# Kernel optimization log

Hardware: AMD Instinct MI355X
Metric: run time of the kernel (lower is better)

The kernel has to match this reference:

```python
import jax, jax.numpy as jnp
import numpy as np

N_V, N_H, T, B = 1024, 512, 128, 256


def setup_inputs() -> dict:
    key = jax.random.key(0)
    k = jax.random.split(key, 3)
    v_data = (jax.random.uniform(k[0], (N_V, T, B)) < 0.5).astype(jnp.float32)  # binary visibles
    W = 0.01 * jax.random.normal(k[1], (N_H, N_V), jnp.float32)
    U = 0.01 * jax.random.normal(k[2], (N_H, N_H), jnp.float32)
    b_h = jnp.zeros((N_H,), jnp.float32)
    b_init = jnp.zeros((N_H,), jnp.float32)
    b_v = jnp.zeros((N_V,), jnp.float32)
    return {"v_data": v_data, "W": W, "U": U, "b_h": b_h, "b_init": b_init,
            "b_v": b_v, "CDk": 2}


def _sample_r_over_time(v, W, U, b_h, b_init):
    # v: (V,T,B) -> r: (H,T,B). Sequential mean-field recurrence over T
    # (RTRBM._sample_r_given_v_over_time: t=0 uses b_init and U=0, t>0 uses U,b_h).
    Wv = jnp.einsum('hv,vtb->thb', W, v)  # (T,H,B)
    r0 = jax.nn.sigmoid(Wv[0] + b_init[:, None])

    def step(r_lag, wv_t):
        r_t = jax.nn.sigmoid(wv_t + U @ r_lag + b_h[:, None])
        return r_t, r_t

    _, rs = jax.lax.scan(step, r0, Wv[1:])
    r = jnp.concatenate([r0[None], rs], axis=0)  # (T,H,B)
    return jnp.transpose(r, (1, 0, 2))  # (H,T,B)


def _parallel_r(v, r_lagged, W, U, b_h, b_init):
    # RTRBM._parallel_sample_r_h_given_v probabilities; v:(V,T,B), r_lagged:(H,T,B)
    r0 = jax.nn.sigmoid(jnp.einsum('hv,vb->hb', W, v[:, 0]) + b_init[:, None])
    rr = jax.nn.sigmoid(jnp.einsum('hv,vtb->htb', W, v[:, 1:])
                        + jnp.einsum('hr,rtb->htb', U, r_lagged[:, :-1])
                        + b_h[:, None, None])
    return jnp.concatenate([r0[:, None], rr], axis=1)  # (H,T,B)


def reference(v_data, W, U, b_h, b_init, b_v, CDk):
    key = jax.random.key(42)
    r_data = _sample_r_over_time(v_data, W, U, b_h, b_init)
    key, sk = jax.random.split(key)
    h_model = jax.random.bernoulli(sk, _parallel_r(v_data, r_data, W, U, b_h, b_init)).astype(v_data.dtype)
    for _ in range(CDk - 1):  # CD-k Gibbs chain (CDk is a concrete Python int)
        key, k1, k2 = jax.random.split(key, 3)
        v_prob = jax.nn.sigmoid(jnp.einsum('hv,htb->vtb', W, h_model) + b_v[:, None, None])
        v_model = jax.random.bernoulli(k1, v_prob).astype(v_data.dtype)
        h_model = jax.random.bernoulli(k2, _parallel_r(v_model, r_data, W, U, b_h, b_init)).astype(v_data.dtype)
    key, kf = jax.random.split(key)
    v_model = jax.random.bernoulli(
        kf, jax.nn.sigmoid(jnp.einsum('hv,htb->vtb', W, h_model) + b_v[:, None, None])
    ).astype(v_data.dtype)
    return (v_model, r_data)
```

## Files before the change

kernel.cpp:

```cpp
#include <hip/hip_runtime.h>
#include <stdint.h>

typedef unsigned long long u64;
typedef uint32_t u32;

#define NV 1024
#define NH 512
#define TT 128
#define BB 256
#define TBsz (TT*BB)
#define HTBsz (NH*TBsz)
#define VTBsz (NV*TBsz)
#define NWV (NV/64)
#define NWH (NH/64)
#define QCAP 1048576u
#define DELTA 5e-4

__host__ __device__ inline void tf2x32(uint32_t k0, uint32_t k1,
                                       uint32_t x0, uint32_t x1,
                                       uint32_t& o0, uint32_t& o1) {
  const uint32_t ks2 = k0 ^ k1 ^ 0x1BD11BDAu;
#define ROTL(x,d) (((x)<<(d))|((x)>>(32-(d))))
#define RND(r) { x0 += x1; x1 = ROTL(x1,r); x1 ^= x0; }
  x0 += k0;  x1 += k1;
  RND(13) RND(15) RND(26) RND(6)
  x0 += k1;  x1 += ks2 + 1u;
  RND(17) RND(29) RND(16) RND(24)
  x0 += ks2; x1 += k0 + 2u;
  RND(13) RND(15) RND(26) RND(6)
  x0 += k0;  x1 += k1 + 3u;
  RND(17) RND(29) RND(16) RND(24)
  x0 += k1;  x1 += ks2 + 4u;
  RND(13) RND(15) RND(26) RND(6)
  x0 += ks2; x1 += k0 + 5u;
  o0 = x0; o1 = x1;
#undef RND
#undef ROTL
}

__device__ inline double tf_uniform64(uint32_t k0, uint32_t k1, uint32_t i) {
  uint32_t o0, o1;
  tf2x32(k0, k1, 0u, i, o0, o1);
  uint32_t bits = o0 ^ o1;
  uint32_t fb = (bits >> 9) | 0x3f800000u;
  float f = __uint_as_float(fb) - 1.0f;
  return (double)f;
}

__device__ inline double sigmoid64(double x) { return 1.0 / (1.0 + exp(-x)); }

__global__ __launch_bounds__(256) void kcvt(const float* __restrict__ s,
                                            double* __restrict__ d, int n) {
  int i = blockIdx.x * 256 + threadIdx.x;
  if (i < n) d[i] = (double)s[i];
}

__global__ __launch_bounds__(256) void kprepU(const float* __restrict__ U,
                                              float4* __restrict__ UB) {
  int i = blockIdx.x * 256 + threadIdx.x;
  int r4 = i / NH;
  int h  = i % NH;
  const float* __restrict__ p = U + (size_t)h*NH + r4*4;
  UB[i] = make_float4(p[0], p[1], p[2], p[3]);
}

__global__ __launch_bounds__(256) void kprepUT(const float* __restrict__ U,
                                               float* __restrict__ UT) {
  int i = blockIdx.x * 256 + threadIdx.x;
  int r = i / NH;
  int h = i % NH;
  UT[i] = U[(size_t)h*NH + r];
}

__global__ __launch_bounds__(256) void kpack_f32(const float* __restrict__ in,
                                                 u64* __restrict__ out) {
  int tb = blockIdx.x * 256 + threadIdx.x;
  for (int w = 0; w < NWV; ++w) {
    u64 m = 0;
    #pragma unroll 8
    for (int j = 0; j < 64; ++j)
      m |= (u64)(in[(size_t)(w*64 + j)*TBsz + tb] != 0.0f ? 1 : 0) << j;
    out[(size_t)tb*NWV + w] = m;
  }
}

__global__ __launch_bounds__(256) void kWv(const u64* __restrict__ vb,
                                           const double* __restrict__ W64,
                                           double* __restrict__ WvT) {
  const int HM = 8;
  int t  = blockIdx.x / (NH/HM);
  int h0 = (blockIdx.x % (NH/HM)) * HM;
  int tb = t*BB + threadIdx.x;
  u64 m[NWV];
  #pragma unroll
  for (int w = 0; w < NWV; ++w) m[w] = vb[(size_t)tb*NWV + w];
  double acc[HM];
  #pragma unroll
  for (int i = 0; i < HM; ++i) acc[i] = 0.0;
  const double2* __restrict__ W2 = (const double2*)W64;
  for (int w = 0; w < NWV; ++w) {
    u64 mw = m[w];
    #pragma unroll 8
    for (int j2 = 0; j2 < 32; ++j2) {
      double bd0 = (double)((unsigned)((mw >> (2*j2+0)) & 1ull));
      double bd1 = (double)((unsigned)((mw >> (2*j2+1)) & 1ull));
      int vi = w*32 + j2;
      #pragma unroll
      for (int i = 0; i < HM; ++i) {
        double2 wv = W2[(size_t)(h0+i)*(NV/2) + vi];
        acc[i] = fma(bd0, wv.x, acc[i]);
        acc[i] = fma(bd1, wv.y, acc[i]);
      }
    }
  }
  #pragma unroll
  for (int i = 0; i < HM; ++i)
    WvT[(size_t)tb*NH + h0 + i] = acc[i];
}

__global__ __launch_bounds__(512) void krecur(const double* __restrict__ WvT,
                                              const float4* __restrict__ UB,
                                              const float* __restrict__ bh,
                                              const float* __restrict__ binit,
                                              double* __restrict__ rT) {
  __shared__ double rA[2][NH];
  const int b = blockIdx.x;
  const int h = threadIdx.x;
  const double bhd = (double)bh[h];
  double p = sigmoid64(WvT[(size_t)b*NH + h] + (double)binit[h]);
  rA[0][h] = p;
  rT[(size_t)b*NH + h] = p;
  __syncthreads();
  int cur = 0;
  for (int t = 1; t < TT; ++t) {
    double acc = WvT[((size_t)t*BB + b)*NH + h];
    double a0=0, a1=0, a2=0, a3=0;
    const double2* __restrict__ rA2 = (const double2*)rA[cur];
    #pragma unroll 4
    for (int r = 0; r < NH; r += 4) {
      float4 u4 = UB[(size_t)(r >> 2)*NH + h];
      double2 q01 = rA2[(r>>1)+0];
      double2 q23 = rA2[(r>>1)+1];
      a0 = fma((double)u4.x, q01.x, a0);
      a1 = fma((double)u4.y, q01.y, a1);
      a2 = fma((double)u4.z, q23.x, a2);
      a3 = fma((double)u4.w, q23.y, a3);
    }
    p = sigmoid64((acc + ((a0+a1)+(a2+a3))) + bhd);
    rA[cur ^ 1][h] = p;
    rT[((size_t)t*BB + b)*NH + h] = p;
    __syncthreads();
    cur ^= 1;
  }
}

__global__ __launch_bounds__(256) void ktrans(const double* __restrict__ rT,
                                              float* __restrict__ out_r) {
  __shared__ double lds[32][33];
  int t  = blockIdx.x;
  int h0 = blockIdx.y * 32;
  int b0 = blockIdx.z * 32;
  int tx = threadIdx.x & 31;
  int ty = threadIdx.x >> 5;
  #pragma unroll
  for (int i = 0; i < 4; ++i) {
    int row = ty*4 + i;
    lds[row][tx] = rT[((size_t)t*BB + b0 + row)*NH + h0 + tx];
  }
  __syncthreads();
  #pragma unroll
  for (int i = 0; i < 4; ++i) {
    int row = ty*4 + i;
    out_r[(size_t)(h0+row)*TBsz + (size_t)t*BB + b0 + tx] = (float)lds[tx][row];
  }
}

__global__ __launch_bounds__(256) void ksample8(const double* __restrict__ rT,
                                                uint8_t* __restrict__ hbytes,
                                                u32 k0, u32 k1) {
  int i  = blockIdx.x * 256 + threadIdx.x;
  int tb = i >> 6;
  int hw = i & 63;
  int t = tb / BB, b = tb % BB;
  const double* __restrict__ rp = rT + ((size_t)t*BB + b)*NH + hw*8;
  unsigned byte = 0;
  #pragma unroll
  for (int j = 0; j < 8; ++j) {
    double p = rp[j];
    double u = tf_uniform64(k0, k1, (u32)((hw*8 + j)*TBsz + tb));
    byte |= (u < p) ? (1u << j) : 0u;
  }
  hbytes[(size_t)tb*(NH/8) + hw] = (uint8_t)byte;
}

__global__ __launch_bounds__(256) void kvis32(
    const float* __restrict__ W, const float* __restrict__ bv,
    const u64* __restrict__ hbits, uint8_t* __restrict__ vbytes,
    float* __restrict__ vf, u32* __restrict__ queue, u32* __restrict__ cnt,
    u32 k0, u32 k1) {
  const int VM = 16;
  int t  = blockIdx.x / (NV/VM);
  int v0 = (blockIdx.x % (NV/VM)) * VM;
  int tb = t*BB + threadIdx.x;
  u64 hb[NWH];
  #pragma unroll
  for (int w = 0; w < NWH; ++w) hb[w] = hbits[(size_t)tb*NWH + w];
  float acc[VM];
  #pragma unroll
  for (int i = 0; i < VM; ++i) acc[i] = 0.f;
  for (int w = 0; w < NWH; ++w) {
    u64 mw = hb[w];
    #pragma unroll 4
    for (int j = 0; j < 64; ++j) {
      float bd = (float)((u32)((mw >> j) & 1ull));
      const float4* __restrict__ Wp4 =
          (const float4*)(W + (size_t)(w*64 + j)*NV + v0);
      float4 w0 = Wp4[0], w1 = Wp4[1], w2 = Wp4[2], w3 = Wp4[3];
      acc[ 0] = fmaf(bd, w0.x, acc[ 0]);
      acc[ 1] = fmaf(bd, w0.y, acc[ 1]);
      acc[ 2] = fmaf(bd, w0.z, acc[ 2]);
      acc[ 3] = fmaf(bd, w0.w, acc[ 3]);
      acc[ 4] = fmaf(bd, w1.x, acc[ 4]);
      acc[ 5] = fmaf(bd, w1.y, acc[ 5]);
      acc[ 6] = fmaf(bd, w1.z, acc[ 6]);
      acc[ 7] = fmaf(bd, w1.w, acc[ 7]);
      acc[ 8] = fmaf(bd, w2.x, acc[ 8]);
      acc[ 9] = fmaf(bd, w2.y, acc[ 9]);
      acc[10] = fmaf(bd, w2.z, acc[10]);
      acc[11] = fmaf(bd, w2.w, acc[11]);
      acc[12] = fmaf(bd, w3.x, acc[12]);
      acc[13] = fmaf(bd, w3.y, acc[13]);
      acc[14] = fmaf(bd, w3.z, acc[14]);
      acc[15] = fmaf(bd, w3.w, acc[15]);
    }
  }
  unsigned bits = 0;
  #pragma unroll
  for (int i = 0; i < VM; ++i) {
    float p = 1.f / (1.f + __expf(-(acc[i] + bv[v0+i])));
    size_t o = (size_t)(v0+i)*TBsz + tb;
    double u = tf_uniform64(k0, k1, (u32)o);
    double diff = (double)p - u;
    unsigned smp = diff > 0.0 ? 1u : 0u;
    if (fabs(diff) < DELTA) {
      u32 s = atomicAdd(cnt, 1u);
      if (s < QCAP) queue[s] = (u32)o;
    }
    bits |= smp << i;
    if (vf) vf[o] = (float)smp;
  }
  if (vbytes)
    *(uint16_t*)(vbytes + (size_t)tb*(NV/8) + (v0 >> 3)) = (uint16_t)bits;
}

__global__ __launch_bounds__(256) void kvis_fix(
    const float* __restrict__ W, const float* __restrict__ bv,
    const u64* __restrict__ hbits, u64* __restrict__ fixbits,
    float* __restrict__ vf, const u32* __restrict__ queue,
    const u32* __restrict__ cnt, u32 k0, u32 k1) {
  u32 n = *cnt; if (n > QCAP) n = QCAP;
  for (u32 q = blockIdx.x*256 + threadIdx.x; q < n; q += gridDim.x*256) {
    u32 o = queue[q];
    u32 v = o / TBsz, tb = o % TBsz;
    double a0=0, a1=0, a2=0, a3=0;
    for (int w = 0; w < NWH; ++w) {
      u64 mw = hbits[(size_t)tb*NWH + w];
      for (int j = 0; j < 64; j += 4) {
        if ((mw >> (j+0)) & 1ull) a0 += (double)W[(size_t)(w*64+j+0)*NV + v];
        if ((mw >> (j+1)) & 1ull) a1 += (double)W[(size_t)(w*64+j+1)*NV + v];
        if ((mw >> (j+2)) & 1ull) a2 += (double)W[(size_t)(w*64+j+2)*NV + v];
        if ((mw >> (j+3)) & 1ull) a3 += (double)W[(size_t)(w*64+j+3)*NV + v];
      }
    }
    double p = sigmoid64(((a0+a1)+(a2+a3)) + (double)bv[v]);
    double u = tf_uniform64(k0, k1, o);
    unsigned smp = (u < p) ? 1u : 0u;
    if (vf) vf[o] = (float)smp;
    if (fixbits) {
      size_t wi = (size_t)tb*NWV + (v >> 6);
      unsigned bit = v & 63u;
      unsigned cur = (unsigned)((fixbits[wi] >> bit) & 1ull);
      if (cur != smp) atomicXor(&fixbits[wi], 1ull << bit);
    }
  }
}

__global__ __launch_bounds__(256) void khid32(
    const u64* __restrict__ vbits, const float* __restrict__ W,
    const float* __restrict__ UT, const float* __restrict__ bh,
    const float* __restrict__ binit, const float* __restrict__ r32,
    uint8_t* __restrict__ hbytes, u32* __restrict__ queue,
    u32* __restrict__ cnt, u32 k0, u32 k1) {
  const int HM = 8;
  int t  = blockIdx.x / (NH/HM);
  int h0 = (blockIdx.x % (NH/HM)) * HM;
  int tb = t*BB + threadIdx.x;
  u64 m[NWV];
  #pragma unroll
  for (int w = 0; w < NWV; ++w) m[w] = vbits[(size_t)tb*NWV + w];
  float acc[HM];
  #pragma unroll
  for (int i = 0; i < HM; ++i) acc[i] = 0.f;
  const float4* __restrict__ W4 = (const float4*)W;
  for (int w = 0; w < NWV; ++w) {
    u64 mw = m[w];
    #pragma unroll 4
    for (int j4 = 0; j4 < 16; ++j4) {
      float bd0 = (float)((u32)((mw >> (4*j4+0)) & 1ull));
      float bd1 = (float)((u32)((mw >> (4*j4+1)) & 1ull));
      float bd2 = (float)((u32)((mw >> (4*j4+2)) & 1ull));
      float bd3 = (float)((u32)((mw >> (4*j4+3)) & 1ull));
      int vi = w*16 + j4;
      #pragma unroll
      for (int i = 0; i < HM; ++i) {
        float4 wv = W4[(size_t)(h0+i)*(NV/4) + vi];
        acc[i] = fmaf(bd0, wv.x, acc[i]);
        acc[i] = fmaf(bd1, wv.y, acc[i]);
        acc[i] = fmaf(bd2, wv.z, acc[i]);
        acc[i] = fmaf(bd3, wv.w, acc[i]);
      }
    }
  }
  if (t > 0) {
    const float* __restrict__ rp = r32 + (size_t)(t-1)*BB + threadIdx.x;
    const float4* __restrict__ UT4 = (const float4*)UT;
    #pragma unroll 4
    for (int r = 0; r < NH; ++r) {
      float rv = rp[(size_t)r*TBsz];
      float4 ua = UT4[(size_t)r*(NH/4) + (h0 >> 2) + 0];
      float4 ub = UT4[(size_t)r*(NH/4) + (h0 >> 2) + 1];
      acc[0] = fmaf(ua.x, rv, acc[0]);
      acc[1] = fmaf(ua.y, rv, acc[1]);
      acc[2] = fmaf(ua.z, rv, acc[2]);
      acc[3] = fmaf(ua.w, rv, acc[3]);
      acc[4] = fmaf(ub.x, rv, acc[4]);
      acc[5] = fmaf(ub.y, rv, acc[5]);
      acc[6] = fmaf(ub.z, rv, acc[6]);
      acc[7] = fmaf(ub.w, rv, acc[7]);
    }
    #pragma unroll
    for (int i = 0; i < HM; ++i) acc[i] += bh[h0+i];
  } else {
    #pragma unroll
    for (int i = 0; i < HM; ++i) acc[i] += binit[h0+i];
  }
  unsigned byte = 0;
  #pragma unroll
  for (int i = 0; i < HM; ++i) {
    float p = 1.f / (1.f + __expf(-acc[i]));
    size_t o = (size_t)(h0+i)*TBsz + tb;
    double u = tf_uniform64(k0, k1, (u32)o);
    double diff = (double)p - u;
    unsigned smp = diff > 0.0 ? 1u : 0u;
    if (fabs(diff) < DELTA) {
      u32 s = atomicAdd(cnt, 1u);
      if (s < QCAP) queue[s] = (u32)o;
    }
    byte |= smp << i;
  }
  hbytes[(size_t)tb*(NH/8) + (h0 >> 3)] = (uint8_t)byte;
}

__global__ __launch_bounds__(256) void khid_fix(
    const u64* __restrict__ vbits, const float* __restrict__ W,
    const double* __restrict__ U64, const float* __restrict__ bh,
    const float* __restrict__ binit, const double* __restrict__ rT,
    u64* __restrict__ fixbits, const u32* __restrict__ queue,
    const u32* __restrict__ cnt, u32 k0, u32 k1) {
  u32 n = *cnt; if (n > QCAP) n = QCAP;
  for (u32 q = blockIdx.x*256 + threadIdx.x; q < n; q += gridDim.x*256) {
    u32 o = queue[q];
    u32 h = o / TBsz, tb = o % TBsz;
    u32 t = tb / BB, b = tb % BB;
    double a0=0, a1=0, a2=0, a3=0;
    for (int w = 0; w < NWV; ++w) {
      u64 mw = vbits[(size_t)tb*NWV + w];
      for (int j = 0; j < 64; j += 4) {
        if ((mw >> (j+0)) & 1ull) a0 += (double)W[(size_t)h*NV + w*64+j+0];
        if ((mw >> (j+1)) & 1ull) a1 += (double)W[(size_t)h*NV + w*64+j+1];
        if ((mw >> (j+2)) & 1ull) a2 += (double)W[(size_t)h*NV + w*64+j+2];
        if ((mw >> (j+3)) & 1ull) a3 += (double)W[(size_t)h*NV + w*64+j+3];
      }
    }
    double logit = (a0+a1) + (a2+a3);
    if (t > 0) {
      const double* __restrict__ rp = rT + ((size_t)(t-1)*BB + b)*NH;
      const double* __restrict__ Ur = U64 + (size_t)h*NH;
      double u0=0, u1=0, u2=0, u3=0;
      for (int r = 0; r < NH; r += 4) {
        u0 = fma(Ur[r+0], rp[r+0], u0);
        u1 = fma(Ur[r+1], rp[r+1], u1);
        u2 = fma(Ur[r+2], rp[r+2], u2);
        u3 = fma(Ur[r+3], rp[r+3], u3);
      }
      logit = (logit + ((u0+u1)+(u2+u3))) + (double)bh[h];
    } else {
      logit += (double)binit[h];
    }
    double p = sigmoid64(logit);
    double u = tf_uniform64(k0, k1, o);
    unsigned smp = (u < p) ? 1u : 0u;
    size_t wi = (size_t)tb*NWH + (h >> 6);
    unsigned bit = h & 63u;
    unsigned cur = (unsigned)((fixbits[wi] >> bit) & 1ull);
    if (cur != smp) atomicXor(&fixbits[wi], 1ull << bit);
  }
}

extern "C" void kernel_launch(void* const* d_in, const int* in_sizes, int n_in,
                              void* d_out, int out_size, void* d_ws, size_t ws_size,
                              hipStream_t stream) {
  const float* vd    = (const float*)d_in[0];
  const float* W     = (const float*)d_in[1];
  const float* U     = (const float*)d_in[2];
  const float* bh    = (const float*)d_in[3];
  const float* binit = (const float*)d_in[4];
  const float* bv    = (const float*)d_in[5];

  float* out_v = (float*)d_out;
  float* out_r = (float*)d_out + VTBsz;
  double* WvT = (double*)d_out;

  char* w = (char*)d_ws;
  double* rT    = (double*)w;  w += (size_t)HTBsz*8;
  u64* vdbits   = (u64*)w;     w += (size_t)TBsz*NWV*8;
  u64* v1bits   = (u64*)w;     w += (size_t)TBsz*NWV*8;
  u64* h1bits   = (u64*)w;     w += (size_t)TBsz*NWH*8;
  u64* h2bits   = (u64*)w;     w += (size_t)TBsz*NWH*8;
  double* W64   = (double*)w;  w += (size_t)NH*NV*8;
  double* U64   = (double*)w;  w += (size_t)NH*NH*8;
  float4* UB    = (float4*)w;  w += (size_t)NH*NH*4;
  float* UT     = (float*)w;   w += (size_t)NH*NH*4;
  u32* q0       = (u32*)w;     w += (size_t)QCAP*4;
  u32* q1       = (u32*)w;     w += (size_t)QCAP*4;
  u32* q2       = (u32*)w;     w += (size_t)QCAP*4;
  u32* cnt      = (u32*)w;     w += 256;
  (void)ws_size; (void)in_sizes; (void)n_in; (void)out_size;

  uint32_t ka0,ka1, sk0,sk1;
  tf2x32(0u,42u, 0u,0u, ka0,ka1);
  tf2x32(0u,42u, 0u,1u, sk0,sk1);
  uint32_t kb0,kb1, k10,k11, k20,k21;
  tf2x32(ka0,ka1, 0u,0u, kb0,kb1);
  tf2x32(ka0,ka1, 0u,1u, k10,k11);
  tf2x32(ka0,ka1, 0u,2u, k20,k21);
  uint32_t kc0,kc1, kf0,kf1;
  tf2x32(kb0,kb1, 0u,0u, kc0,kc1);
  tf2x32(kb0,kb1, 0u,1u, kf0,kf1);

  hipMemsetAsync(cnt, 0, 3*sizeof(u32), stream);

  kcvt<<<(NH*NV+255)/256, 256, 0, stream>>>(W, W64, NH*NV);
  kcvt<<<(NH*NH+255)/256, 256, 0, stream>>>(U, U64, NH*NH);
  kprepU<<<(NH*NH/4)/256, 256, 0, stream>>>(U, UB);
  kprepUT<<<(NH*NH)/256, 256, 0, stream>>>(U, UT);
  kpack_f32<<<TBsz/256, 256, 0, stream>>>(vd, vdbits);

  kWv<<<TT*(NH/8), 256, 0, stream>>>(vdbits, W64, WvT);

  krecur<<<BB, NH, 0, stream>>>(WvT, UB, bh, binit, rT);

  ktrans<<<dim3(TT, NH/32, BB/32), 256, 0, stream>>>(rT, out_r);

  ksample8<<<(TBsz*64)/256, 256, 0, stream>>>(rT, (uint8_t*)h1bits, sk0, sk1);

  kvis32<<<TT*(NV/16), 256, 0, stream>>>(W, bv, h1bits, (uint8_t*)v1bits, nullptr,
                                         q0, cnt+0, k10, k11);
  kvis_fix<<<128, 256, 0, stream>>>(W, bv, h1bits, v1bits, nullptr,
                                    q0, cnt+0, k10, k11);

  khid32<<<TT*(NH/8), 256, 0, stream>>>(v1bits, W, UT, bh, binit, out_r,
                                        (uint8_t*)h2bits, q1, cnt+1, k20, k21);
  khid_fix<<<128, 256, 0, stream>>>(v1bits, W, U64, bh, binit, rT,
                                    h2bits, q1, cnt+1, k20, k21);

  kvis32<<<TT*(NV/16), 256, 0, stream>>>(W, bv, h2bits, nullptr, out_v,
                                         q2, cnt+2, kf0, kf1);
  kvis_fix<<<128, 256, 0, stream>>>(W, bv, h2bits, nullptr, out_v,
                                    q2, cnt+2, kf0, kf1);
}
```

Baseline: 4.982 ms.

## Use split-bf16 MFMA for visible pass, fuse h-sampling into transpose, cache U in registers

The visible-layer matvec is replaced with an MFMA bf16 GEMM. W is split into hi and lo bf16 parts and hidden bits are expanded into a swizzled LDS tile, replacing the scalar per-thread FMA loop over W. Hidden sampling is folded into the transpose kernel so rT is not re-read. The recurrence kernel keeps a quarter of U in registers to cut global loads per step. The split-bf16 product carries a small precision loss, which the existing near-threshold fix-up queue is meant to absorb.

Measured after the change: 5.709 ms. 14.6% more time.

```diff
diff --git a/kernel.cpp b/kernel.cpp
--- a/kernel.cpp
+++ b/kernel.cpp
@@ -1,8 +1,11 @@
 #include <hip/hip_runtime.h>
+#include <hip/hip_bf16.h>
 #include <stdint.h>
 
 typedef unsigned long long u64;
 typedef uint32_t u32;
+typedef __attribute__((ext_vector_type(8))) short bf16x8;
+typedef __attribute__((ext_vector_type(4))) float f32x4;
 
 #define NV 1024
 #define NH 512
@@ -72,6 +75,24 @@
   UT[i] = U[(size_t)h*NH + r];
 }
 
+__global__ __launch_bounds__(256) void kprepA(const float* __restrict__ W,
+                                              ushort* __restrict__ A1,
+                                              ushort* __restrict__ A2) {
+  int idx = blockIdx.x * 256 + threadIdx.x;
+  int i    = idx & 7;
+  int lane = (idx >> 3) & 63;
+  int ks   = (idx >> 9) & 15;
+  int vt   = idx >> 13;
+  int h = ks*32 + ((lane >> 4) << 3) + i;
+  int v = vt*16 + (lane & 15);
+  float w = W[(size_t)h*NV + v];
+  __hip_bfloat16 b1 = __float2bfloat16(w);
+  float r = w - __bfloat162float(b1);
+  __hip_bfloat16 b2 = __float2bfloat16(r);
+  A1[idx] = *reinterpret_cast<ushort*>(&b1);
+  A2[idx] = *reinterpret_cast<ushort*>(&b2);
+}
+
 __global__ __launch_bounds__(256) void kpack_f32(const float* __restrict__ in,
                                                  u64* __restrict__ out) {
   int tb = blockIdx.x * 256 + threadIdx.x;
@@ -127,6 +148,9 @@
   const int b = blockIdx.x;
   const int h = threadIdx.x;
   const double bhd = (double)bh[h];
+  float4 ureg[32];
+  #pragma unroll
+  for (int i = 0; i < 32; ++i) ureg[i] = UB[(size_t)i*NH + h];
   double p = sigmoid64(WvT[(size_t)b*NH + h] + (double)binit[h]);
   rA[0][h] = p;
   rT[(size_t)b*NH + h] = p;
@@ -136,8 +160,18 @@
     double acc = WvT[((size_t)t*BB + b)*NH + h];
     double a0=0, a1=0, a2=0, a3=0;
     const double2* __restrict__ rA2 = (const double2*)rA[cur];
+    #pragma unroll 8
+    for (int r = 0; r < 128; r += 4) {
+      float4 u4 = ureg[r >> 2];
+      double2 q01 = rA2[(r>>1)+0];
+      double2 q23 = rA2[(r>>1)+1];
+      a0 = fma((double)u4.x, q01.x, a0);
+      a1 = fma((double)u4.y, q01.y, a1);
+      a2 = fma((double)u4.z, q23.x, a2);
+      a3 = fma((double)u4.w, q23.y, a3);
+    }
     #pragma unroll 4
-    for (int r = 0; r < NH; r += 4) {
+    for (int r = 128; r < NH; r += 4) {
       float4 u4 = UB[(size_t)(r >> 2)*NH + h];
       double2 q01 = rA2[(r>>1)+0];
       double2 q23 = rA2[(r>>1)+1];
@@ -154,8 +188,10 @@
   }
 }
 
-__global__ __launch_bounds__(256) void ktrans(const double* __restrict__ rT,
-                                              float* __restrict__ out_r) {
+__global__ __launch_bounds__(256) void ktrans_s(const double* __restrict__ rT,
+                                                float* __restrict__ out_r,
+                                                uint8_t* __restrict__ hbytes,
+                                                u32 k0, u32 k1) {
   __shared__ double lds[32][33];
   int t  = blockIdx.x;
   int h0 = blockIdx.y * 32;
@@ -173,84 +209,117 @@
     int row = ty*4 + i;
     out_r[(size_t)(h0+row)*TBsz + (size_t)t*BB + b0 + tx] = (float)lds[tx][row];
   }
-}
-
-__global__ __launch_bounds__(256) void ksample8(const double* __restrict__ rT,
-                                                uint8_t* __restrict__ hbytes,
-                                                u32 k0, u32 k1) {
-  int i  = blockIdx.x * 256 + threadIdx.x;
-  int tb = i >> 6;
-  int hw = i & 63;
-  int t = tb / BB, b = tb % BB;
-  const double* __restrict__ rp = rT + ((size_t)t*BB + b)*NH + hw*8;
-  unsigned byte = 0;
-  #pragma unroll
-  for (int j = 0; j < 8; ++j) {
-    double p = rp[j];
-    double u = tf_uniform64(k0, k1, (u32)((hw*8 + j)*TBsz + tb));
-    byte |= (u < p) ? (1u << j) : 0u;
-  }
-  hbytes[(size_t)tb*(NH/8) + hw] = (uint8_t)byte;
-}
-
-__global__ __launch_bounds__(256) void kvis32(
-    const float* __restrict__ W, const float* __restrict__ bv,
-    const u64* __restrict__ hbits, uint8_t* __restrict__ vbytes,
-    float* __restrict__ vf, u32* __restrict__ queue, u32* __restrict__ cnt,
-    u32 k0, u32 k1) {
-  const int VM = 16;
-  int t  = blockIdx.x / (NV/VM);
-  int v0 = (blockIdx.x % (NV/VM)) * VM;
-  int tb = t*BB + threadIdx.x;
-  u64 hb[NWH];
-  #pragma unroll
-  for (int w = 0; w < NWH; ++w) hb[w] = hbits[(size_t)tb*NWH + w];
-  float acc[VM];
-  #pragma unroll
-  for (int i = 0; i < VM; ++i) acc[i] = 0.f;
-  for (int w = 0; w < NWH; ++w) {
-    u64 mw = hb[w];
-    #pragma unroll 4
-    for (int j = 0; j < 64; ++j) {
-      float bd = (float)((u32)((mw >> j) & 1ull));
-      const float4* __restrict__ Wp4 =
-          (const float4*)(W + (size_t)(w*64 + j)*NV + v0);
-      float4 w0 = Wp4[0], w1 = Wp4[1], w2 = Wp4[2], w3 = Wp4[3];
-      acc[ 0] = fmaf(bd, w0.x, acc[ 0]);
-      acc[ 1] = fmaf(bd, w0.y, acc[ 1]);
-      acc[ 2] = fmaf(bd, w0.z, acc[ 2]);
-      acc[ 3] = fmaf(bd, w0.w, acc[ 3]);
-      acc[ 4] = fmaf(bd, w1.x, acc[ 4]);
-      acc[ 5] = fmaf(bd, w1.y, acc[ 5]);
-      acc[ 6] = fmaf(bd, w1.z, acc[ 6]);
-      acc[ 7] = fmaf(bd, w1.w, acc[ 7]);
-      acc[ 8] = fmaf(bd, w2.x, acc[ 8]);
-      acc[ 9] = fmaf(bd, w2.y, acc[ 9]);
-      acc[10] = fmaf(bd, w2.z, acc[10]);
-      acc[11] = fmaf(bd, w2.w, acc[11]);
-      acc[12] = fmaf(bd, w3.x, acc[12]);
-      acc[13] = fmaf(bd, w3.y, acc[13]);
-      acc[14] = fmaf(bd, w3.z, acc[14]);
-      acc[15] = fmaf(bd, w3.w, acc[15]);
-    }
-  }
-  unsigned bits = 0;
-  #pragma unroll
-  for (int i = 0; i < VM; ++i) {
-    float p = 1.f / (1.f + __expf(-(acc[i] + bv[v0+i])));
-    size_t o = (size_t)(v0+i)*TBsz + tb;
-    double u = tf_uniform64(k0, k1, (u32)o);
-    double diff = (double)p - u;
-    unsigned smp = diff > 0.0 ? 1u : 0u;
-    if (fabs(diff) < DELTA) {
-      u32 s = atomicAdd(cnt, 1u);
-      if (s < QCAP) queue[s] = (u32)o;
-    }
-    bits |= smp << i;
-    if (vf) vf[o] = (float)smp;
-  }
-  if (vbytes)
-    *(uint16_t*)(vbytes + (size_t)tb*(NV/8) + (v0 >> 3)) = (uint16_t)bits;
+  if (threadIdx.x < 128) {
+    int tbr = threadIdx.x >> 2;
+    int bix = threadIdx.x & 3;
+    int tb  = t*BB + b0 + tbr;
+    unsigned byte = 0;
+    #pragma unroll
+    for (int j = 0; j < 8; ++j) {
+      int hrel = bix*8 + j;
+      double p = lds[tbr][hrel];
+      double u = tf_uniform64(k0, k1, (u32)((h0 + hrel)*TBsz + tb));
+      byte |= (u < p) ? (1u << j) : 0u;
+    }
+    hbytes[(size_t)tb*(NH/8) + (h0 >> 3) + bix] = (uint8_t)byte;
+  }
+}
+
+__global__ __launch_bounds__(256) void kvisM(
+    const ushort* __restrict__ A1, const ushort* __restrict__ A2,
+    const float* __restrict__ bv, const u64* __restrict__ hbits,
+    u64* __restrict__ vbits, float* __restrict__ vf,
+    u32* __restrict__ queue, u32* __restrict__ cnt, u32 k0, u32 k1) {
+  __shared__ ushort Blds[64*512];
+  int nblk = blockIdx.x & 511;
+  int vblk = blockIdx.x >> 9;
+  int tb0 = nblk * 64, v0 = vblk * 64;
+  int tid = threadIdx.x;
+  {
+    int c = tid >> 2, seg = tid & 3;
+    const u64* hp = hbits + (size_t)(tb0 + c)*NWH + seg*2;
+    #pragma unroll
+    for (int half = 0; half < 2; ++half) {
+      u64 mm = hp[half];
+      int kbase = seg*128 + half*64;
+      #pragma unroll
+      for (int j2 = 0; j2 < 32; ++j2) {
+        int k = kbase + 2*j2;
+        u32 val = (u32)((mm >> (2*j2)) & 1ull) * 0x3F80u
+                | (u32)((mm >> (2*j2+1)) & 1ull) * 0x3F800000u;
+        int blk = (k >> 3) ^ (c & 7);
+        *(u32*)&Blds[c*512 + (blk << 3) + (k & 7)] = val;
+      }
+    }
+  }
+  __syncthreads();
+  int wv = tid >> 6, l = tid & 63;
+  int wr = wv >> 1, wc = wv & 1;
+  f32x4 acc[2][2];
+  #pragma unroll
+  for (int m = 0; m < 2; ++m)
+    #pragma unroll
+    for (int n = 0; n < 2; ++n) acc[m][n] = (f32x4){0.f,0.f,0.f,0.f};
+  for (int ks = 0; ks < 16; ++ks) {
+    bf16x8 bf[2];
+    #pragma unroll
+    for (int n = 0; n < 2; ++n) {
+      int col = wc*32 + n*16 + (l & 15);
+      int k = ks*32 + ((l >> 4) << 3);
+      int blk = (k >> 3) ^ (col & 7);
+      bf[n] = *(const bf16x8*)&Blds[col*512 + (blk << 3)];
+    }
+    #pragma unroll
+    for (int m = 0; m < 2; ++m) {
+      int vt = vblk*4 + wr*2 + m;
+      size_t abase = (((size_t)vt*16 + ks)*64 + l)*8;
+      bf16x8 a1 = *(const bf16x8*)&A1[abase];
+      bf16x8 a2 = *(const bf16x8*)&A2[abase];
+      #pragma unroll
+      for (int n = 0; n < 2; ++n) {
+        acc[m][n] = __builtin_amdgcn_mfma_f32_16x16x32_bf16(a1, bf[n], acc[m][n], 0,0,0);
+        acc[m][n] = __builtin_amdgcn_mfma_f32_16x16x32_bf16(a2, bf[n], acc[m][n], 0,0,0);
+      }
+    }
+  }
+  u64 mask[2] = {0, 0};
+  int coln[2];
+  #pragma unroll
+  for (int n = 0; n < 2; ++n) {
+    int col = wc*32 + n*16 + (l & 15);
+    coln[n] = col;
+    int tb = tb0 + col;
+    #pragma unroll
+    for (int m = 0; m < 2; ++m) {
+      #pragma unroll
+      for (int r = 0; r < 4; ++r) {
+        int vrel = wr*32 + m*16 + ((l >> 4) << 2) + r;
+        int v = v0 + vrel;
+        float p = 1.f / (1.f + __expf(-(acc[m][n][r] + bv[v])));
+        size_t o = (size_t)v*TBsz + tb;
+        double u = tf_uniform64(k0, k1, (u32)o);
+        double diff = (double)p - u;
+        unsigned smp = diff > 0.0 ? 1u : 0u;
+        if (fabs(diff) < DELTA) {
+          u32 s = atomicAdd(cnt, 1u);
+          if (s < QCAP) queue[s] = (u32)o;
+        }
+        if (smp) mask[n] |= 1ull << vrel;
+        if (vf) vf[o] = (float)smp;
+      }
+    }
+  }
+  if (vbits) {
+    __syncthreads();
+    u64* sbits = (u64*)Blds;
+    if (tid < 64) sbits[tid] = 0;
+    __syncthreads();
+    atomicOr(&sbits[coln[0]], mask[0]);
+    atomicOr(&sbits[coln[1]], mask[1]);
+    __syncthreads();
+    if (tid < 64)
+      vbits[(size_t)(tb0 + tid)*NWV + (v0 >> 6)] = sbits[tid];
+  }
 }
 
 __global__ __launch_bounds__(256) void kvis_fix(
@@ -431,6 +500,8 @@
   double* U64   = (double*)w;  w += (size_t)NH*NH*8;
   float4* UB    = (float4*)w;  w += (size_t)NH*NH*4;
   float* UT     = (float*)w;   w += (size_t)NH*NH*4;
+  ushort* A1    = (ushort*)w;  w += (size_t)NH*NV*2;
+  ushort* A2    = (ushort*)w;  w += (size_t)NH*NV*2;
   u32* q0       = (u32*)w;     w += (size_t)QCAP*4;
   u32* q1       = (u32*)w;     w += (size_t)QCAP*4;
   u32* q2       = (u32*)w;     w += (size_t)QCAP*4;
@@ -454,18 +525,18 @@
   kcvt<<<(NH*NH+255)/256, 256, 0, stream>>>(U, U64, NH*NH);
   kprepU<<<(NH*NH/4)/256, 256, 0, stream>>>(U, UB);
   kprepUT<<<(NH*NH)/256, 256, 0, stream>>>(U, UT);
+  kprepA<<<(NH*NV)/256, 256, 0, stream>>>(W, A1, A2);
   kpack_f32<<<TBsz/256, 256, 0, stream>>>(vd, vdbits);
 
   kWv<<<TT*(NH/8), 256, 0, stream>>>(vdbits, W64, WvT);
 
   krecur<<<BB, NH, 0, stream>>>(WvT, UB, bh, binit, rT);
 
-  ktrans<<<dim3(TT, NH/32, BB/32), 256, 0, stream>>>(rT, out_r);
-
-  ksample8<<<(TBsz*64)/256, 256, 0, stream>>>(rT, (uint8_t*)h1bits, sk0, sk1);
-
-  kvis32<<<TT*(NV/16), 256, 0, stream>>>(W, bv, h1bits, (uint8_t*)v1bits, nullptr,
-                                         q0, cnt+0, k10, k11);
+  ktrans_s<<<dim3(TT, NH/32, BB/32), 256, 0, stream>>>(rT, out_r,
+                                                       (uint8_t*)h1bits, sk0, sk1);
+
+  kvisM<<<16*512, 256, 0, stream>>>(A1, A2, bv, h1bits, v1bits, nullptr,
+                                    q0, cnt+0, k10, k11);
   kvis_fix<<<128, 256, 0, stream>>>(W, bv, h1bits, v1bits, nullptr,
                                     q0, cnt+0, k10, k11);
 
@@ -474,8 +545,8 @@
   khid_fix<<<128, 256, 0, stream>>>(v1bits, W, U64, bh, binit, rT,
                                     h2bits, q1, cnt+1, k20, k21);
 
-  kvis32<<<TT*(NV/16), 256, 0, stream>>>(W, bv, h2bits, nullptr, out_v,
-                                         q2, cnt+2, kf0, kf1);
+  kvisM<<<16*512, 256, 0, stream>>>(A1, A2, bv, h2bits, nullptr, out_v,
+                                    q2, cnt+2, kf0, kf1);
   kvis_fix<<<128, 256, 0, stream>>>(W, bv, h2bits, nullptr, out_v,
                                     q2, cnt+2, kf0, kf1);
 }
```
